# Kernel tuning notes

Hardware: AMD Instinct MI355X
Metric: run time of the kernel (lower is better)

The kernel has to match this reference:

```python
import jax, jax.numpy as jnp
import numpy as np

B, T, C = 8, 1024, 768
H, D = 12, 64

def setup_inputs() -> dict:
    key = jax.random.key(0)
    ks = jax.random.split(key, 6)
    s = 0.02
    return {
        "x": jax.random.normal(ks[0], (B, T, C), dtype=jnp.float32),
        "Wq": jax.random.normal(ks[1], (H, C, D), dtype=jnp.float32) * s,
        "Wk": jax.random.normal(ks[2], (H, C, D), dtype=jnp.float32) * s,
        "Wv": jax.random.normal(ks[3], (H, C, D), dtype=jnp.float32) * s,
        "Wproj": jax.random.normal(ks[4], (C, C), dtype=jnp.float32) * s,
        "bproj": jnp.zeros((C,), dtype=jnp.float32),
    }

def reference(x, Wq, Wk, Wv, Wproj, bproj):
    # per-head projections, vectorized over heads: [B,H,T,D]
    q = jnp.einsum('btc,hcd->bhtd', x, Wq)
    k = jnp.einsum('btc,hcd->bhtd', x, Wk)
    v = jnp.einsum('btc,hcd->bhtd', x, Wv)
    scale = 1.0 / jnp.sqrt(jnp.asarray(q.shape[-1], q.dtype))
    scores = jnp.einsum('bhtd,bhsd->bhts', q, k) * scale  # [B,H,T,T]
    attn = jax.nn.softmax(scores, axis=-1)
    out = jnp.einsum('bhts,bhsd->bhtd', attn, v)          # [B,H,T,D]
    # concat heads along last dim -> [B,T,H*D]
    out = out.transpose(0, 2, 1, 3).reshape(x.shape[0], x.shape[1], -1)
    return out @ Wproj + bproj
```

## Files before the change

kernel.cpp:

```cpp
#include <hip/hip_runtime.h>
#include <hip/hip_bf16.h>

using u16 = unsigned short;

typedef __attribute__((ext_vector_type(8))) short bf16x8;
typedef __attribute__((ext_vector_type(4))) float f32x4;
typedef __attribute__((ext_vector_type(16))) float f32x16;

#define B_ 8
#define T_ 1024
#define C_ 768
#define H_ 12
#define D_ 64

typedef const void __attribute__((address_space(1))) gv_t;
typedef void __attribute__((address_space(3))) lv_t;

__device__ __forceinline__ void gload_lds16(const void* g, void* l) {
  __builtin_amdgcn_global_load_lds((gv_t*)g, (lv_t*)l, 16, 0, 0);
}

__device__ __forceinline__ u16 f2b(float f) {
  union { float f; unsigned u; } a; a.f = f;
  unsigned r = a.u + 0x7FFFu + ((a.u >> 16) & 1u);
  return (u16)(r >> 16);
}

__device__ __forceinline__ float fexp2(float x) {
  float r;
  asm("v_exp_f32 %0, %1" : "=v"(r) : "v"(x));
  return r;
}

__device__ __forceinline__ unsigned cvtpk_bf16(float lo, float hi) {
  unsigned r;
  asm("v_cvt_pk_bf16_f32 %0, %1, %2" : "=v"(r) : "v"(lo), "v"(hi));
  return r;
}
__device__ __forceinline__ void plane32_swap(unsigned &a, unsigned &b) {
  asm volatile("v_permlane32_swap_b32 %0, %1" : "+v"(a), "+v"(b));
}

__global__ __launch_bounds__(256) void prep_all(
    const float* __restrict__ x,
    const float* __restrict__ Wq, const float* __restrict__ Wk,
    const float* __restrict__ Wv, const float* __restrict__ Wp,
    u16* __restrict__ Xb, u16* __restrict__ Wqkvt, u16* __restrict__ Wpt)
{
  int bb = blockIdx.x;
  if (bb < 3072) {
    int i = (bb * 256 + threadIdx.x) * 8;
    float4 a = *(const float4*)(x + i);
    float4 b = *(const float4*)(x + i + 4);
    union { bf16x8 v; u16 s[8]; } o;
    o.s[0] = f2b(a.x); o.s[1] = f2b(a.y); o.s[2] = f2b(a.z); o.s[3] = f2b(a.w);
    o.s[4] = f2b(b.x); o.s[5] = f2b(b.y); o.s[6] = f2b(b.z); o.s[7] = f2b(b.w);
    *(bf16x8*)(Xb + i) = o.v;
  } else {
    int idx = (bb - 3072) * 256 + threadIdx.x;
    int p = idx / 589824;
    int r = idx - p * 589824;
    int n = r / 768, c = r - n * 768;
    if (p < 3) {
      const float* W = (p == 0) ? Wq : ((p == 1) ? Wk : Wv);
      int h = n >> 6, d = n & 63;
      Wqkvt[idx] = f2b(W[(size_t)h * (C_ * D_) + (size_t)c * D_ + d]);
    } else {
      Wpt[r] = f2b(Wp[(size_t)c * 768 + n]);
    }
  }
}

#define GEMM_MAINLOOP(APTR, BPTR, KDIM)                                          \
  for (int k0 = 0; k0 < (KDIM); k0 += 64) {                                      \
    _Pragma("unroll")                                                            \
    for (int q = 0; q < 4; ++q) {                                                \
      int db = q * 4096 + t * 16;                                                \
      int row = db >> 7;                                                         \
      int cb = (db ^ ((row & 7) << 4)) & 127;                                    \
      gload_lds16((const char*)(APTR) + ((size_t)(m0 + row) * (KDIM) + k0) * 2 + cb, \
                  (char*)As + db);                                               \
      gload_lds16((const char*)(BPTR) + ((size_t)(n0 + row) * (KDIM) + k0) * 2 + cb, \
                  (char*)Bs + db);                                               \
    }                                                                            \
    asm volatile("s_waitcnt vmcnt(0)" ::: "memory");                             \
    __syncthreads();                                                             \
    _Pragma("unroll")                                                            \
    for (int kq = 0; kq < 2; ++kq) {                                             \
      bf16x8 af[4], bfr[4];                                                      \
      _Pragma("unroll")                                                          \
      for (int i = 0; i < 4; ++i) {                                              \
        int ra = wr + i * 16 + lr;                                               \
        int Ua = ra * 128 + kq * 64 + hc;                                        \
        af[i] = *(const bf16x8*)((const char*)As + (Ua ^ ((ra & 7) << 4)));      \
        int rb = wc + i * 16 + lr;                                               \
        int Ub = rb * 128 + kq * 64 + hc;                                        \
        bfr[i] = *(const bf16x8*)((const char*)Bs + (Ub ^ ((rb & 7) << 4)));     \
      }                                                                          \
      _Pragma("unroll")                                                          \
      for (int i = 0; i < 4; ++i)                                                \
        _Pragma("unroll")                                                        \
        for (int j = 0; j < 4; ++j)                                              \
          acc[i][j] = __builtin_amdgcn_mfma_f32_16x16x32_bf16(af[i], bfr[j],     \
                                                              acc[i][j], 0, 0, 0); \
    }                                                                            \
    __syncthreads();                                                             \
  }

__global__ __launch_bounds__(256) void gemm_qkv(
    const u16* __restrict__ X, const u16* __restrict__ Wt,
    u16* __restrict__ Qw, u16* __restrict__ Kw, u16* __restrict__ Vt)
{
  __shared__ __align__(16) u16 As[128 * 64];
  __shared__ __align__(16) u16 Bs[128 * 64];
  const int t = threadIdx.x;
  const int l = t & 63, w = t >> 6;
  const int lr = l & 15;
  const int hc = (l >> 4) * 16;
  const int m0 = blockIdx.x * 128;
  const int n0 = blockIdx.y * 128;
  const int wr = (w >> 1) * 64, wc = (w & 1) * 64;

  f32x4 acc[4][4] = {};
  GEMM_MAINLOOP(X, Wt, 768)

  #pragma unroll
  for (int j = 0; j < 4; ++j) {
    int col_g = n0 + wc + j * 16 + lr;
    int p = (col_g >= 1536) ? 2 : ((col_g >= 768) ? 1 : 0);
    int rr = col_g - p * 768;
    int h = rr >> 6, d = rr & 63;
    #pragma unroll
    for (int i = 0; i < 4; ++i) {
      int rg0 = m0 + wr + i * 16 + ((l >> 4) << 2);
      int b = rg0 >> 10, tt = rg0 & 1023;
      if (p == 0) {
        size_t base = (((size_t)b * H_ + h) * T_ + tt) * D_ + d;
        #pragma unroll
        for (int r = 0; r < 4; ++r)
          Qw[base + (size_t)r * D_] = f2b(acc[i][j][r] * 0.18033688f);
      } else if (p == 1) {
        size_t base = (((size_t)b * H_ + h) * T_ + tt) * D_ + d;
        #pragma unroll
        for (int r = 0; r < 4; ++r) Kw[base + (size_t)r * D_] = f2b(acc[i][j][r]);
      } else {
        unsigned long long pk =
            (unsigned long long)f2b(acc[i][j][0]) |
            ((unsigned long long)f2b(acc[i][j][1]) << 16) |
            ((unsigned long long)f2b(acc[i][j][2]) << 32) |
            ((unsigned long long)f2b(acc[i][j][3]) << 48);
        *reinterpret_cast<unsigned long long*>(
            &Vt[(((size_t)b * H_ + h) * D_ + d) * T_ + tt]) = pk;
      }
    }
  }
}

__global__ __launch_bounds__(256) void gemm_proj(
    const u16* __restrict__ A, const u16* __restrict__ Wt,
    const float* __restrict__ bias, float* __restrict__ O)
{
  __shared__ __align__(16) u16 As[128 * 64];
  __shared__ __align__(16) u16 Bs[128 * 64];
  const int t = threadIdx.x;
  const int l = t & 63, w = t >> 6;
  const int lr = l & 15;
  const int hc = (l >> 4) * 16;
  const int m0 = blockIdx.x * 128;
  const int n0 = blockIdx.y * 128;
  const int wr = (w >> 1) * 64, wc = (w & 1) * 64;

  f32x4 acc[4][4] = {};
  GEMM_MAINLOOP(A, Wt, 768)

  #pragma unroll
  for (int j = 0; j < 4; ++j) {
    int col_g = n0 + wc + j * 16 + lr;
    float bb = bias[col_g];
    #pragma unroll
    for (int i = 0; i < 4; ++i) {
      int rg0 = m0 + wr + i * 16 + ((l >> 4) << 2);
      #pragma unroll
      for (int r = 0; r < 4; ++r)
        O[(size_t)(rg0 + r) * C_ + col_g] = acc[i][j][r] + bb;
    }
  }
}

__global__ __launch_bounds__(256) void attn_fwd(
    const u16* __restrict__ Qw, const u16* __restrict__ Kw,
    const u16* __restrict__ VT, u16* __restrict__ AO)
{
  __shared__ __align__(16) u16 Ks[2][64 * 64];
  __shared__ __align__(16) u16 Vs[3][64 * 64];
  const int t = threadIdx.x, l = t & 63;
  const int lq = l & 31, lh = l >> 5;

  const int bid = blockIdx.x;
  const int bh = (bid & 7) * 12 + ((bid >> 3) >> 3);
  const int qt = (bid >> 3) & 7;
  const int b = bh / H_, h = bh - b * H_;
  const u16* Qh = Qw + (size_t)bh * (T_ * D_);
  const char* Kp = (const char*)(Kw + (size_t)bh * (T_ * D_));
  const char* Vp = (const char*)(VT + (size_t)bh * (D_ * T_));
  const int q0w = qt * 128 + (t >> 6) * 32;
  const int qrow = q0w + lq;

  bf16x8 qf[4];
  #pragma unroll
  for (int ks = 0; ks < 4; ++ks)
    qf[ks] = *(const bf16x8*)(Qh + (size_t)qrow * D_ + lh * 8 + ks * 16);

  bf16x8 ones;
  {
    union { u16 s[8]; bf16x8 v; } u;
    #pragma unroll
    for (int j = 0; j < 8; ++j) u.s[j] = 0x3F80;
    ones = u.v;
  }

  f32x16 oA = {}, oB = {}, lacc = {};
  bf16x8 pbP[4];

  const int db0 = t * 16, db1 = 4096 + t * 16;
  const int row0 = db0 >> 7, row1 = db1 >> 7;
  const int cb0 = (db0 ^ ((row0 & 7) << 4)) & 127;
  const int cb1 = (db1 ^ ((row1 & 7) << 4)) & 127;

#define ISSUE_TILE(KT, KB, VB)                                                   \
  gload_lds16(Kp + (size_t)((KT) + row0) * 128 + cb0, (char*)Ks[KB] + db0);      \
  gload_lds16(Kp + (size_t)((KT) + row1) * 128 + cb1, (char*)Ks[KB] + db1);      \
  gload_lds16(Vp + (size_t)row0 * 2048 + (KT) * 2 + cb0, (char*)Vs[VB] + db0);   \
  gload_lds16(Vp + (size_t)row1 * 2048 + (KT) * 2 + cb1, (char*)Vs[VB] + db1);

  ISSUE_TILE(0, 0, 0)

  int wv = 1, pv = 2;

  for (int kt_i = 0; kt_i < 16; ++kt_i) {
    const int cur = kt_i & 1;
    asm volatile("s_waitcnt vmcnt(0)" ::: "memory");
    __syncthreads();
    if (kt_i < 15) { ISSUE_TILE((kt_i + 1) * 64, cur ^ 1, wv) }

    f32x16 sA = {}, sB = {};
    {
      bf16x8 ka[4];
      #pragma unroll
      for (int ks = 0; ks < 4; ++ks) {
        int row = lq;
        int U = row * 128 + ks * 32 + lh * 16;
        ka[ks] = *(const bf16x8*)((const char*)Ks[cur] + (U ^ ((row & 7) << 4)));
      }
      #pragma unroll
      for (int ks = 0; ks < 4; ++ks)
        sA = __builtin_amdgcn_mfma_f32_32x32x16_bf16(ka[ks], qf[ks], sA, 0, 0, 0);
      #pragma unroll
      for (int ks = 0; ks < 4; ++ks) {
        int row = lq + 32;
        int U = row * 128 + ks * 32 + lh * 16;
        ka[ks] = *(const bf16x8*)((const char*)Ks[cur] + (U ^ ((row & 7) << 4)));
      }
      #pragma unroll
      for (int ks = 0; ks < 4; ++ks)
        sB = __builtin_amdgcn_mfma_f32_32x32x16_bf16(ka[ks], qf[ks], sB, 0, 0, 0);
    }

    if (kt_i > 0) {
      const char* Vb = (const char*)Vs[pv];
      bf16x8 va[4];
      #pragma unroll
      for (int ks = 0; ks < 4; ++ks) {
        int row = lq;
        int U = row * 128 + ks * 32 + lh * 16;
        va[ks] = *(const bf16x8*)(Vb + (U ^ ((row & 7) << 4)));
      }
      #pragma unroll
      for (int ks = 0; ks < 4; ++ks)
        oA = __builtin_amdgcn_mfma_f32_32x32x16_bf16(va[ks], pbP[ks], oA, 0, 0, 0);
      #pragma unroll
      for (int ks = 0; ks < 4; ++ks) {
        int row = lq + 32;
        int U = row * 128 + ks * 32 + lh * 16;
        va[ks] = *(const bf16x8*)(Vb + (U ^ ((row & 7) << 4)));
      }
      #pragma unroll
      for (int ks = 0; ks < 4; ++ks)
        oB = __builtin_amdgcn_mfma_f32_32x32x16_bf16(va[ks], pbP[ks], oB, 0, 0, 0);
      #pragma unroll
      for (int ks = 0; ks < 4; ++ks)
        lacc = __builtin_amdgcn_mfma_f32_32x32x16_bf16(ones, pbP[ks], lacc, 0, 0, 0);
    }

    #pragma unroll
    for (int r = 0; r < 16; ++r) {
      sA[r] = fexp2(sA[r]);
      sB[r] = fexp2(sB[r]);
    }

    #pragma unroll
    for (int ks = 0; ks < 4; ++ks) {
      f32x16& S = (ks < 2) ? sA : sB;
      const int g = (ks & 1) * 8;
      unsigned a0 = cvtpk_bf16(S[g + 0], S[g + 1]);
      unsigned a1 = cvtpk_bf16(S[g + 2], S[g + 3]);
      unsigned b0 = cvtpk_bf16(S[g + 4], S[g + 5]);
      unsigned b1 = cvtpk_bf16(S[g + 6], S[g + 7]);
      plane32_swap(a0, b0);
      plane32_swap(a1, b1);
      union { unsigned wd[4]; bf16x8 v; } u;
      u.wd[0] = a0; u.wd[1] = a1; u.wd[2] = b0; u.wd[3] = b1;
      pbP[ks] = u.v;
    }

    wv = (wv == 2) ? 0 : wv + 1;
    pv = (pv == 2) ? 0 : pv + 1;
  }
#undef ISSUE_TILE

  {
    const char* Vb = (const char*)Vs[pv];
    bf16x8 va[4];
    #pragma unroll
    for (int ks = 0; ks < 4; ++ks) {
      int row = lq;
      int U = row * 128 + ks * 32 + lh * 16;
      va[ks] = *(const bf16x8*)(Vb + (U ^ ((row & 7) << 4)));
    }
    #pragma unroll
    for (int ks = 0; ks < 4; ++ks)
      oA = __builtin_amdgcn_mfma_f32_32x32x16_bf16(va[ks], pbP[ks], oA, 0, 0, 0);
    #pragma unroll
    for (int ks = 0; ks < 4; ++ks) {
      int row = lq + 32;
      int U = row * 128 + ks * 32 + lh * 16;
      va[ks] = *(const bf16x8*)(Vb + (U ^ ((row & 7) << 4)));
    }
    #pragma unroll
    for (int ks = 0; ks < 4; ++ks)
      oB = __builtin_amdgcn_mfma_f32_32x32x16_bf16(va[ks], pbP[ks], oB, 0, 0, 0);
    #pragma unroll
    for (int ks = 0; ks < 4; ++ks)
      lacc = __builtin_amdgcn_mfma_f32_32x32x16_bf16(ones, pbP[ks], lacc, 0, 0, 0);
  }

  float inv = 1.0f / lacc[0];
  size_t base = ((size_t)b * T_ + qrow) * C_ + h * D_;
  #pragma unroll
  for (int dh = 0; dh < 2; ++dh) {
    const f32x16& OO = dh ? oB : oA;
    #pragma unroll
    for (int g = 0; g < 4; ++g) {
      int d0 = 8 * g + 4 * lh + 32 * dh;
      unsigned long long pk =
          (unsigned long long)f2b(OO[4 * g + 0] * inv) |
          ((unsigned long long)f2b(OO[4 * g + 1] * inv) << 16) |
          ((unsigned long long)f2b(OO[4 * g + 2] * inv) << 32) |
          ((unsigned long long)f2b(OO[4 * g + 3] * inv) << 48);
      *reinterpret_cast<unsigned long long*>(&AO[base + d0]) = pk;
    }
  }
}

extern "C" void kernel_launch(void* const* d_in, const int* in_sizes, int n_in,
                              void* d_out, int out_size, void* d_ws, size_t ws_size,
                              hipStream_t stream) {
  (void)in_sizes; (void)n_in; (void)out_size;
  const float* x     = (const float*)d_in[0];
  const float* Wq    = (const float*)d_in[1];
  const float* Wk    = (const float*)d_in[2];
  const float* Wv    = (const float*)d_in[3];
  const float* Wproj = (const float*)d_in[4];
  const float* bproj = (const float*)d_in[5];

  const size_t NEEDED = 55050240;
  if (ws_size < NEEDED) return;

  char* ws = (char*)d_ws;
  u16* Wpt   = (u16*)(ws);
  u16* Qw    = (u16*)(ws + 1179648);
  u16* Kw    = (u16*)(ws + 13762560);
  u16* Vt    = (u16*)(ws + 26345472);
  u16* Xb    = (u16*)(ws + 38928384);
  u16* AO    = (u16*)(ws + 38928384);
  u16* Wqkvt = (u16*)(ws + 51511296);

  prep_all<<<dim3(12288), dim3(256), 0, stream>>>(x, Wq, Wk, Wv, Wproj, Xb, Wqkvt, Wpt);
  gemm_qkv<<<dim3(64, 18), dim3(256), 0, stream>>>(Xb, Wqkvt, Qw, Kw, Vt);
  attn_fwd<<<dim3(768), dim3(256), 0, stream>>>(Qw, Kw, Vt, AO);
  gemm_proj<<<dim3(64, 6), dim3(256), 0, stream>>>(AO, Wpt, bproj, (float*)d_out);
}
```

Baseline: 132.9 us.

## Double-buffer LDS tiles in GEMM main loop to overlap loads with MFMA

Restructures the shared GEMM main loop to use two LDS buffers per operand. The first K-tile is preloaded, and each iteration issues async global-to-LDS loads for the next tile before computing on the current one. This is meant to hide global memory latency behind MFMA work and removes the trailing barrier per iteration. In exchange, LDS usage per block doubles, which can lower occupancy.

New measurement: 142.1 us. +6.9%, slower.

```diff
diff --git a/kernel.cpp b/kernel.cpp
--- a/kernel.cpp
+++ b/kernel.cpp
@@ -72,47 +72,66 @@
 }
 
 #define GEMM_MAINLOOP(APTR, BPTR, KDIM)                                          \
-  for (int k0 = 0; k0 < (KDIM); k0 += 64) {                                      \
+  {                                                                              \
     _Pragma("unroll")                                                            \
     for (int q = 0; q < 4; ++q) {                                                \
       int db = q * 4096 + t * 16;                                                \
       int row = db >> 7;                                                         \
       int cb = (db ^ ((row & 7) << 4)) & 127;                                    \
-      gload_lds16((const char*)(APTR) + ((size_t)(m0 + row) * (KDIM) + k0) * 2 + cb, \
+      gload_lds16((const char*)(APTR) + ((size_t)(m0 + row) * (KDIM)) * 2 + cb,  \
                   (char*)As + db);                                               \
-      gload_lds16((const char*)(BPTR) + ((size_t)(n0 + row) * (KDIM) + k0) * 2 + cb, \
+      gload_lds16((const char*)(BPTR) + ((size_t)(n0 + row) * (KDIM)) * 2 + cb,  \
                   (char*)Bs + db);                                               \
     }                                                                            \
-    asm volatile("s_waitcnt vmcnt(0)" ::: "memory");                             \
-    __syncthreads();                                                             \
-    _Pragma("unroll")                                                            \
-    for (int kq = 0; kq < 2; ++kq) {                                             \
-      bf16x8 af[4], bfr[4];                                                      \
+    const int NIT = (KDIM) / 64;                                                 \
+    for (int it = 0; it < NIT; ++it) {                                           \
+      const int cur = it & 1;                                                    \
+      asm volatile("s_waitcnt vmcnt(0)" ::: "memory");                           \
+      __syncthreads();                                                           \
+      if (it + 1 < NIT) {                                                        \
+        int k0 = (it + 1) * 64;                                                  \
+        int nb = (cur ^ 1) * 16384;                                              \
+        _Pragma("unroll")                                                        \
+        for (int q = 0; q < 4; ++q) {                                            \
+          int db = q * 4096 + t * 16;                                            \
+          int row = db >> 7;                                                     \
+          int cb = (db ^ ((row & 7) << 4)) & 127;                                \
+          gload_lds16((const char*)(APTR) + ((size_t)(m0 + row) * (KDIM) + k0) * 2 + cb, \
+                      (char*)As + nb + db);                                      \
+          gload_lds16((const char*)(BPTR) + ((size_t)(n0 + row) * (KDIM) + k0) * 2 + cb, \
+                      (char*)Bs + nb + db);                                      \
+        }                                                                        \
+      }                                                                          \
+      const char* Ab = (const char*)As + cur * 16384;                            \
+      const char* Bb = (const char*)Bs + cur * 16384;                            \
       _Pragma("unroll")                                                          \
-      for (int i = 0; i < 4; ++i) {                                              \
-        int ra = wr + i * 16 + lr;                                               \
-        int Ua = ra * 128 + kq * 64 + hc;                                        \
-        af[i] = *(const bf16x8*)((const char*)As + (Ua ^ ((ra & 7) << 4)));      \
-        int rb = wc + i * 16 + lr;                                               \
-        int Ub = rb * 128 + kq * 64 + hc;                                        \
-        bfr[i] = *(const bf16x8*)((const char*)Bs + (Ub ^ ((rb & 7) << 4)));     \
+      for (int kq = 0; kq < 2; ++kq) {                                           \
+        bf16x8 af[4], bfr[4];                                                    \
+        _Pragma("unroll")                                                        \
+        for (int i = 0; i < 4; ++i) {                                            \
+          int ra = wr + i * 16 + lr;                                             \
+          int Ua = ra * 128 + kq * 64 + hc;                                      \
+          af[i] = *(const bf16x8*)(Ab + (Ua ^ ((ra & 7) << 4)));                 \
+          int rb = wc + i * 16 + lr;                                             \
+          int Ub = rb * 128 + kq * 64 + hc;                                      \
+          bfr[i] = *(const bf16x8*)(Bb + (Ub ^ ((rb & 7) << 4)));                \
+        }                                                                        \
+        _Pragma("unroll")                                                        \
+        for (int i = 0; i < 4; ++i)                                              \
+          _Pragma("unroll")                                                      \
+          for (int j = 0; j < 4; ++j)                                            \
+            acc[i][j] = __builtin_amdgcn_mfma_f32_16x16x32_bf16(af[i], bfr[j],   \
+                                                                acc[i][j], 0, 0, 0); \
       }                                                                          \
-      _Pragma("unroll")                                                          \
-      for (int i = 0; i < 4; ++i)                                                \
-        _Pragma("unroll")                                                        \
-        for (int j = 0; j < 4; ++j)                                              \
-          acc[i][j] = __builtin_amdgcn_mfma_f32_16x16x32_bf16(af[i], bfr[j],     \
-                                                              acc[i][j], 0, 0, 0); \
     }                                                                            \
-    __syncthreads();                                                             \
   }
 
 __global__ __launch_bounds__(256) void gemm_qkv(
     const u16* __restrict__ X, const u16* __restrict__ Wt,
     u16* __restrict__ Qw, u16* __restrict__ Kw, u16* __restrict__ Vt)
 {
-  __shared__ __align__(16) u16 As[128 * 64];
-  __shared__ __align__(16) u16 Bs[128 * 64];
+  __shared__ __align__(16) u16 As[2 * 128 * 64];
+  __shared__ __align__(16) u16 Bs[2 * 128 * 64];
   const int t = threadIdx.x;
   const int l = t & 63, w = t >> 6;
   const int lr = l & 15;
@@ -160,8 +179,8 @@
     const u16* __restrict__ A, const u16* __restrict__ Wt,
     const float* __restrict__ bias, float* __restrict__ O)
 {
-  __shared__ __align__(16) u16 As[128 * 64];
-  __shared__ __align__(16) u16 Bs[128 * 64];
+  __shared__ __align__(16) u16 As[2 * 128 * 64];
+  __shared__ __align__(16) u16 Bs[2 * 128 * 64];
   const int t = threadIdx.x;
   const int l = t & 63, w = t >> 6;
   const int lr = l & 15;
```

## Double-buffer GEMM LDS tiles with K=32 steps and vectorize weight transpose

Applied to the files above, without the earlier changes.

The shared GEMM main loop now splits K into 32-wide tiles held in two LDS buffers. The next tile's global-to-LDS loads are issued before the MFMAs on the current tile, which overlaps memory latency with compute and removes one barrier per step. The cost is more iterations, each with a wait and a barrier, and a smaller per-step MFMA batch that may hide less latency. Separately, the weight-prep path reads float4s and writes four transposed bf16 values per thread, cutting the prep grid size. Its scattered 2-byte stores stay uncoalesced.

Result: no change. 133.4 us (+0.4%).

```diff
diff --git a/kernel.cpp b/kernel.cpp
--- a/kernel.cpp
+++ b/kernel.cpp
@@ -58,44 +58,74 @@
     *(bf16x8*)(Xb + i) = o.v;
   } else {
     int idx = (bb - 3072) * 256 + threadIdx.x;
-    int p = idx / 589824;
-    int r = idx - p * 589824;
-    int n = r / 768, c = r - n * 768;
+    int p = idx / 147456;
+    int r = idx - p * 147456;
     if (p < 3) {
       const float* W = (p == 0) ? Wq : ((p == 1) ? Wk : Wv);
-      int h = n >> 6, d = n & 63;
-      Wqkvt[idx] = f2b(W[(size_t)h * (C_ * D_) + (size_t)c * D_ + d]);
+      int d4 = r & 15;
+      int c  = (r >> 4) % 768;
+      int h  = r / 12288;
+      float4 v = *(const float4*)(W + (size_t)h * 49152 + (size_t)c * 64 + d4 * 4);
+      size_t nb = (size_t)p * 589824 + ((size_t)h * 64 + d4 * 4) * 768 + c;
+      Wqkvt[nb]           = f2b(v.x);
+      Wqkvt[nb + 768]     = f2b(v.y);
+      Wqkvt[nb + 1536]    = f2b(v.z);
+      Wqkvt[nb + 2304]    = f2b(v.w);
     } else {
-      Wpt[r] = f2b(Wp[(size_t)c * 768 + n]);
+      int co4 = r % 192;
+      int ci  = r / 192;
+      float4 v = *(const float4*)(Wp + (size_t)ci * 768 + co4 * 4);
+      size_t ob = (size_t)(co4 * 4) * 768 + ci;
+      Wpt[ob]        = f2b(v.x);
+      Wpt[ob + 768]  = f2b(v.y);
+      Wpt[ob + 1536] = f2b(v.z);
+      Wpt[ob + 2304] = f2b(v.w);
     }
   }
 }
 
 #define GEMM_MAINLOOP(APTR, BPTR, KDIM)                                          \
-  for (int k0 = 0; k0 < (KDIM); k0 += 64) {                                      \
+  {                                                                              \
     _Pragma("unroll")                                                            \
-    for (int q = 0; q < 4; ++q) {                                                \
+    for (int q = 0; q < 2; ++q) {                                                \
       int db = q * 4096 + t * 16;                                                \
-      int row = db >> 7;                                                         \
-      int cb = (db ^ ((row & 7) << 4)) & 127;                                    \
-      gload_lds16((const char*)(APTR) + ((size_t)(m0 + row) * (KDIM) + k0) * 2 + cb, \
+      int row = db >> 6;                                                         \
+      int cb = (db ^ ((row & 3) << 4)) & 63;                                     \
+      gload_lds16((const char*)(APTR) + ((size_t)(m0 + row) * (KDIM)) * 2 + cb,  \
                   (char*)As + db);                                               \
-      gload_lds16((const char*)(BPTR) + ((size_t)(n0 + row) * (KDIM) + k0) * 2 + cb, \
+      gload_lds16((const char*)(BPTR) + ((size_t)(n0 + row) * (KDIM)) * 2 + cb,  \
                   (char*)Bs + db);                                               \
     }                                                                            \
-    asm volatile("s_waitcnt vmcnt(0)" ::: "memory");                             \
-    __syncthreads();                                                             \
-    _Pragma("unroll")                                                            \
-    for (int kq = 0; kq < 2; ++kq) {                                             \
+    const int NIT = (KDIM) / 32;                                                 \
+    for (int it = 0; it < NIT; ++it) {                                           \
+      const int cur = it & 1;                                                    \
+      asm volatile("s_waitcnt vmcnt(0)" ::: "memory");                           \
+      __syncthreads();                                                           \
+      if (it + 1 < NIT) {                                                        \
+        int k0 = (it + 1) * 32;                                                  \
+        int nb = (cur ^ 1) * 8192;                                               \
+        _Pragma("unroll")                                                        \
+        for (int q = 0; q < 2; ++q) {                                            \
+          int db = q * 4096 + t * 16;                                            \
+          int row = db >> 6;                                                     \
+          int cb = (db ^ ((row & 3) << 4)) & 63;                                 \
+          gload_lds16((const char*)(APTR) + ((size_t)(m0 + row) * (KDIM) + k0) * 2 + cb, \
+                      (char*)As + nb + db);                                      \
+          gload_lds16((const char*)(BPTR) + ((size_t)(n0 + row) * (KDIM) + k0) * 2 + cb, \
+                      (char*)Bs + nb + db);                                      \
+        }                                                                        \
+      }                                                                          \
+      const char* Ab = (const char*)As + cur * 8192;                             \
+      const char* Bb = (const char*)Bs + cur * 8192;                             \
       bf16x8 af[4], bfr[4];                                                      \
       _Pragma("unroll")                                                          \
       for (int i = 0; i < 4; ++i) {                                              \
         int ra = wr + i * 16 + lr;                                               \
-        int Ua = ra * 128 + kq * 64 + hc;                                        \
-        af[i] = *(const bf16x8*)((const char*)As + (Ua ^ ((ra & 7) << 4)));      \
+        int Ua = ra * 64 + hc;                                                   \
+        af[i] = *(const bf16x8*)(Ab + (Ua ^ ((ra & 3) << 4)));                   \
         int rb = wc + i * 16 + lr;                                               \
-        int Ub = rb * 128 + kq * 64 + hc;                                        \
-        bfr[i] = *(const bf16x8*)((const char*)Bs + (Ub ^ ((rb & 7) << 4)));     \
+        int Ub = rb * 64 + hc;                                                   \
+        bfr[i] = *(const bf16x8*)(Bb + (Ub ^ ((rb & 3) << 4)));                  \
       }                                                                          \
       _Pragma("unroll")                                                          \
       for (int i = 0; i < 4; ++i)                                                \
@@ -104,15 +134,14 @@
           acc[i][j] = __builtin_amdgcn_mfma_f32_16x16x32_bf16(af[i], bfr[j],     \
                                                               acc[i][j], 0, 0, 0); \
     }                                                                            \
-    __syncthreads();                                                             \
   }
 
 __global__ __launch_bounds__(256) void gemm_qkv(
     const u16* __restrict__ X, const u16* __restrict__ Wt,
     u16* __restrict__ Qw, u16* __restrict__ Kw, u16* __restrict__ Vt)
 {
-  __shared__ __align__(16) u16 As[128 * 64];
-  __shared__ __align__(16) u16 Bs[128 * 64];
+  __shared__ __align__(16) u16 As[2 * 128 * 32];
+  __shared__ __align__(16) u16 Bs[2 * 128 * 32];
   const int t = threadIdx.x;
   const int l = t & 63, w = t >> 6;
   const int lr = l & 15;
@@ -160,8 +189,8 @@
     const u16* __restrict__ A, const u16* __restrict__ Wt,
     const float* __restrict__ bias, float* __restrict__ O)
 {
-  __shared__ __align__(16) u16 As[128 * 64];
-  __shared__ __align__(16) u16 Bs[128 * 64];
+  __shared__ __align__(16) u16 As[2 * 128 * 32];
+  __shared__ __align__(16) u16 Bs[2 * 128 * 32];
   const int t = threadIdx.x;
   const int l = t & 63, w = t >> 6;
   const int lr = l & 15;
@@ -385,7 +414,7 @@
   u16* AO    = (u16*)(ws + 38928384);
   u16* Wqkvt = (u16*)(ws + 51511296);
 
-  prep_all<<<dim3(12288), dim3(256), 0, stream>>>(x, Wq, Wk, Wv, Wproj, Xb, Wqkvt, Wpt);
+  prep_all<<<dim3(5376), dim3(256), 0, stream>>>(x, Wq, Wk, Wv, Wproj, Xb, Wqkvt, Wpt);
   gemm_qkv<<<dim3(64, 18), dim3(256), 0, stream>>>(Xb, Wqkvt, Qw, Kw, Vt);
   attn_fwd<<<dim3(768), dim3(256), 0, stream>>>(Qw, Kw, Vt, AO);
   gemm_proj<<<dim3(64, 6), dim3(256), 0, stream>>>(AO, Wpt, bproj, (float*)d_out);
```
